# Kernel tuning notes

Measured on AMD Instinct MI355X. Metric: run time of the kernel, lower is better.

## Reference

```python
import jax, jax.numpy as jnp
import numpy as np

D_MODEL = 1024
NHEAD = 16
DK = D_MODEL // NHEAD
B, LQ, LK = 4, 2048, 2048


def setup_inputs() -> dict:
    key = jax.random.key(0)
    ks = jax.random.split(key, 11)
    s = 1.0 / np.sqrt(D_MODEL)
    inp = {
        "q": jax.random.normal(ks[0], (B, LQ, D_MODEL), jnp.float32),
        "k": jax.random.normal(ks[1], (B, LK, D_MODEL), jnp.float32),
        "v": jax.random.normal(ks[2], (B, LK, D_MODEL), jnp.float32),
        "attn_mask": jnp.triu(jnp.ones((LQ, LK), dtype=bool), k=1),  # True = masked (causal)
        "Wq": jax.random.normal(ks[3], (D_MODEL, D_MODEL), jnp.float32) * s,
        "bq": jnp.zeros((D_MODEL,), jnp.float32),
        "Wk": jax.random.normal(ks[4], (D_MODEL, D_MODEL), jnp.float32) * s,
        "bk": jnp.zeros((D_MODEL,), jnp.float32),
        "Wv": jax.random.normal(ks[5], (D_MODEL, D_MODEL), jnp.float32) * s,
        "bv": jnp.zeros((D_MODEL,), jnp.float32),
        "Wo": jax.random.normal(ks[6], (D_MODEL, D_MODEL), jnp.float32) * s,
        "bo": jnp.zeros((D_MODEL,), jnp.float32),
    }
    return inp


def _split_heads(x, L):
    # (B, L, D) -> (B, H, L, dk)
    return x.reshape(B, L, NHEAD, DK).transpose(0, 2, 1, 3)


def reference(q, k, v, attn_mask, Wq, bq, Wk, bk, Wv, bv, Wo, bo):
    qh = _split_heads(q @ Wq + bq, LQ)
    kh = _split_heads(k @ Wk + bk, LK)
    vh = _split_heads(v @ Wv + bv, LK)
    scale = 1.0 / np.sqrt(DK).astype(np.float32)
    scores = jnp.einsum("bhqd,bhkd->bhqk", qh, kh) * scale
    scores = jnp.where(attn_mask[None, None, :, :], -jnp.inf, scores)
    attn = jax.nn.softmax(scores, axis=-1)
    ctx = jnp.einsum("bhqk,bhkd->bhqd", attn, vh)
    ctx = ctx.transpose(0, 2, 1, 3).reshape(B, LQ, D_MODEL)
    return ctx @ Wo + bo
```

## Files before the change

kernel.cpp:

```cpp
#include <hip/hip_runtime.h>

#define D_MODEL 1024
#define NHEAD 16
#define DKH 64
#define BATCH 4
#define SEQ 2048
#define MROWS (BATCH*SEQ)

typedef unsigned short u16;
typedef __attribute__((ext_vector_type(8))) short bf16x8;
typedef __attribute__((ext_vector_type(4))) float f32x4;

__device__ __forceinline__ u16 f2bf(float f) {
  union { float f; unsigned int u; } x; x.f = f;
  unsigned int r = x.u + 0x7FFFu + ((x.u >> 16) & 1u);
  return (u16)(r >> 16);
}
__device__ __forceinline__ u16 f2bf_fast(float f) {
  union { float f; unsigned int u; } x; x.f = f;
  return (u16)((x.u + 0x7FFFu) >> 16);
}

__device__ __forceinline__ f32x4 mfma16(bf16x8 a, bf16x8 b, f32x4 c) {
  return __builtin_amdgcn_mfma_f32_16x16x32_bf16(a, b, c, 0, 0, 0);
}

__device__ __forceinline__ void gld_lds16(const void* g, void* l) {
  __builtin_amdgcn_global_load_lds((const __attribute__((address_space(1))) unsigned int*)g,
                                   (__attribute__((address_space(3))) unsigned int*)l, 16, 0, 0);
}

__global__ __launch_bounds__(256) void cvt3_kernel(
    const float* __restrict__ q, const float* __restrict__ k, const float* __restrict__ v,
    u16* __restrict__ oq, u16* __restrict__ ok, u16* __restrict__ ov) {
  const int seg = blockIdx.y;
  const float* in = (seg == 0) ? q : (seg == 1) ? k : v;
  u16* out = (seg == 0) ? oq : (seg == 1) ? ok : ov;
  int i = (blockIdx.x * 256 + threadIdx.x) * 4;
  float4 vv = *(const float4*)(in + i);
  ushort4 o;
  o.x = f2bf(vv.x); o.y = f2bf(vv.y); o.z = f2bf(vv.z); o.w = f2bf(vv.w);
  *(ushort4*)(out + i) = o;
}

__global__ __launch_bounds__(256) void transpose_cvt4(
    const float* __restrict__ W0, const float* __restrict__ W1,
    const float* __restrict__ W2, const float* __restrict__ W3,
    u16* __restrict__ T0, u16* __restrict__ T1,
    u16* __restrict__ T2, u16* __restrict__ T3) {
  const int z = blockIdx.z;
  const float* W = (z == 0) ? W0 : (z == 1) ? W1 : (z == 2) ? W2 : W3;
  u16* Wt = (z == 0) ? T0 : (z == 1) ? T1 : (z == 2) ? T2 : T3;
  __shared__ float tile[32][33];
  int bx = blockIdx.x * 32, by = blockIdx.y * 32;
  int tx = threadIdx.x, ty = threadIdx.y;
#pragma unroll
  for (int j = 0; j < 32; j += 8)
    tile[ty + j][tx] = W[(size_t)(by + ty + j) * D_MODEL + bx + tx];
  __syncthreads();
#pragma unroll
  for (int j = 0; j < 32; j += 8)
    Wt[(size_t)(bx + ty + j) * D_MODEL + by + tx] = f2bf(tile[tx][ty + j]);
}

__global__ __launch_bounds__(256, 2) void gemm_qkv_kernel(
    const u16* __restrict__ Aq, const u16* __restrict__ Ak, const u16* __restrict__ Av,
    const u16* __restrict__ Wt,
    const float* __restrict__ bq, const float* __restrict__ bk, const float* __restrict__ bv,
    u16* __restrict__ Qhd, u16* __restrict__ Khd, u16* __restrict__ Vhd, float qscale) {
  __shared__ u16 As[128 * 32];
  __shared__ u16 Bs[128 * 32];
  const int tid = threadIdx.x;
  const int lane = tid & 63;
  const int w = tid >> 6;
  const int wr = w >> 1, wc = w & 1;
  const int lo = lane & 15, g = lane >> 4;

  const int flat = blockIdx.x;
  const int swzb = (flat & 7) * 192 + (flat >> 3);
  const int m0 = (swzb / 24) * 128;
  const int n0 = (swzb % 24) * 128;
  const int chunk = n0 >> 10;
  const u16* A = (chunk == 0) ? Aq : (chunk == 1) ? Ak : Av;
  const float* bias = (chunk == 0) ? bq : (chunk == 1) ? bk : bv;
  const float scale = (chunk == 0) ? qscale : 1.0f;

  f32x4 acc[4][4] = {};

  for (int k0 = 0; k0 < D_MODEL; k0 += 32) {
#pragma unroll
    for (int cc = 0; cc < 2; ++cc) {
      int t = (w * 2 + cc) * 64 + lane;
      gld_lds16(A + (size_t)(m0 + (t >> 2)) * D_MODEL + k0 + (t & 3) * 8,
                As + (size_t)(w * 2 + cc) * 512);
      gld_lds16(Wt + (size_t)(n0 + (t >> 2)) * D_MODEL + k0 + (t & 3) * 8,
                Bs + (size_t)(w * 2 + cc) * 512);
    }
    __syncthreads();
    bf16x8 af[4], bf[4];
#pragma unroll
    for (int m = 0; m < 4; ++m)
      af[m] = *(const bf16x8*)&As[(wr * 64 + m * 16 + lo) * 32 + g * 8];
#pragma unroll
    for (int n = 0; n < 4; ++n)
      bf[n] = *(const bf16x8*)&Bs[(wc * 64 + n * 16 + lo) * 32 + g * 8];
#pragma unroll
    for (int m = 0; m < 4; ++m)
#pragma unroll
      for (int n = 0; n < 4; ++n)
        acc[m][n] = mfma16(af[m], bf[n], acc[m][n]);
    __syncthreads();
  }

#pragma unroll
  for (int m = 0; m < 4; ++m)
#pragma unroll
    for (int n = 0; n < 4; ++n) {
      int row0 = m0 + wr * 64 + m * 16 + g * 4;
      int colc = (n0 & 1023) + wc * 64 + n * 16 + lo;
      int hh = colc >> 6, d = colc & 63;
      int bb = row0 >> 11;
      float v0 = (acc[m][n][0] + bias[colc]) * scale;
      float v1 = (acc[m][n][1] + bias[colc]) * scale;
      float v2 = (acc[m][n][2] + bias[colc]) * scale;
      float v3 = (acc[m][n][3] + bias[colc]) * scale;
      if (chunk < 2) {
        u16* out = chunk ? Khd : Qhd;
#pragma unroll
        for (int i = 0; i < 4; ++i) {
          int l = (row0 + i) & 2047;
          float vi = (i == 0) ? v0 : (i == 1) ? v1 : (i == 2) ? v2 : v3;
          out[(((size_t)(bb * NHEAD + hh)) * SEQ + l) * DKH + d] = f2bf(vi);
        }
      } else {
        int l = row0 & 2047;
        int kh = (l >> 2) & 7;
        int pos = (l & ~31) | ((2 * (kh & 3) + (kh >> 2)) << 2);
        ushort4 o;
        o.x = f2bf(v0); o.y = f2bf(v1); o.z = f2bf(v2); o.w = f2bf(v3);
        *(ushort4*)&Vhd[(((size_t)(bb * NHEAD + hh)) * DKH + d) * SEQ + pos] = o;
      }
    }
}

__global__ __launch_bounds__(256, 2) void gemm_o_kernel(
    const u16* __restrict__ A, const u16* __restrict__ Bt,
    const float* __restrict__ bias, float* __restrict__ Cout) {
  __shared__ u16 As[128 * 32];
  __shared__ u16 Bs[128 * 32];
  const int tid = threadIdx.x;
  const int lane = tid & 63;
  const int w = tid >> 6;
  const int wr = w >> 1, wc = w & 1;
  const int lo = lane & 15, g = lane >> 4;

  const int flat = blockIdx.x;
  const int swzb = (flat & 7) * 64 + (flat >> 3);
  const int m0 = (swzb >> 3) * 128;
  const int n0 = (swzb & 7) * 128;

  f32x4 acc[4][4] = {};

  for (int k0 = 0; k0 < D_MODEL; k0 += 32) {
#pragma unroll
    for (int cc = 0; cc < 2; ++cc) {
      int t = (w * 2 + cc) * 64 + lane;
      gld_lds16(A + (size_t)(m0 + (t >> 2)) * D_MODEL + k0 + (t & 3) * 8,
                As + (size_t)(w * 2 + cc) * 512);
      gld_lds16(Bt + (size_t)(n0 + (t >> 2)) * D_MODEL + k0 + (t & 3) * 8,
                Bs + (size_t)(w * 2 + cc) * 512);
    }
    __syncthreads();
    bf16x8 af[4], bf[4];
#pragma unroll
    for (int m = 0; m < 4; ++m)
      af[m] = *(const bf16x8*)&As[(wr * 64 + m * 16 + lo) * 32 + g * 8];
#pragma unroll
    for (int n = 0; n < 4; ++n)
      bf[n] = *(const bf16x8*)&Bs[(wc * 64 + n * 16 + lo) * 32 + g * 8];
#pragma unroll
    for (int m = 0; m < 4; ++m)
#pragma unroll
      for (int n = 0; n < 4; ++n)
        acc[m][n] = mfma16(af[m], bf[n], acc[m][n]);
    __syncthreads();
  }

#pragma unroll
  for (int m = 0; m < 4; ++m)
#pragma unroll
    for (int n = 0; n < 4; ++n) {
      int row0 = m0 + wr * 64 + m * 16 + g * 4;
      int col = n0 + wc * 64 + n * 16 + lo;
#pragma unroll
      for (int i = 0; i < 4; ++i)
        Cout[(size_t)(row0 + i) * D_MODEL + col] = acc[m][n][i] + bias[col];
    }
}

__global__ __launch_bounds__(256, 3) void attn_kernel(
    const u16* __restrict__ Qh, const u16* __restrict__ Kh,
    const u16* __restrict__ Vt, u16* __restrict__ ctx) {
  const int blk = blockIdx.x;
  const int xcd = blk & 7;
  const int local = blk >> 3;
  const int qb = 15 - (local >> 3);
  const int head = xcd * 8 + (local & 7);
  const int b = head >> 4, h = head & (NHEAD - 1);

  const int tid = threadIdx.x;
  const int lane = tid & 63;
  const int w = tid >> 6;
  const int lo = lane & 15, g = lane >> 4;
  const int swz = (lo & 7) << 4;

  __shared__ u16 Ks[3][64 * 64];
  __shared__ u16 Vs[3][64 * 64];

  const size_t hoff = ((size_t)(b * NHEAD + h)) * SEQ * DKH;
  const u16* Qp = Qh + hoff;
  const u16* Kp = Kh + hoff;
  const u16* Vp = Vt + hoff;

  const int nt = 2 * qb + 2;
  const int qmin = qb * 128 + w * 32;

  bf16x8 aq[2][2];
#pragma unroll
  for (int qs = 0; qs < 2; ++qs)
#pragma unroll
    for (int cc = 0; cc < 2; ++cc)
      aq[qs][cc] = *(const bf16x8*)(Qp + (size_t)(qmin + qs * 16 + lo) * DKH + cc * 32 + g * 8);

  const int r_lo = lane >> 3;
  const int sgr = (lane & 7) ^ r_lo;

  auto STAGE = [&](int buf, int t64) {
#pragma unroll
    for (int j = 0; j < 2; ++j) {
      int row = w * 16 + j * 8 + r_lo;
      gld_lds16(Kp + (size_t)(t64 * 64 + row) * DKH + sgr * 8, &Ks[buf][(w * 2 + j) * 512]);
      gld_lds16(Vp + (size_t)row * SEQ + t64 * 64 + sgr * 8, &Vs[buf][(w * 2 + j) * 512]);
    }
  };

  STAGE(0, 0);
  STAGE(1, 1);
  asm volatile("s_waitcnt vmcnt(0)" ::: "memory");
  __builtin_amdgcn_s_barrier();

  f32x4 c[2][4] = {};
  float m_run[2] = {-1e30f, -1e30f}, l_run[2] = {0.f, 0.f};
  int cur = 0;

  for (int kt = 0; kt < nt; ++kt) {
    int b2 = cur + 2; if (b2 >= 3) b2 -= 3;
    if (kt + 2 < nt) STAGE(b2, kt + 2);

    f32x4 s[2][4] = {};
#pragma unroll
    for (int kn = 0; kn < 4; ++kn) {
      const char* krow = (const char*)&Ks[cur][(kn * 16 + lo) * 64];
#pragma unroll
      for (int cc = 0; cc < 2; ++cc) {
        bf16x8 ak = *(const bf16x8*)(krow + ((cc * 64 + g * 16) ^ swz));
        s[0][kn] = mfma16(ak, aq[0][cc], s[0][kn]);
        s[1][kn] = mfma16(ak, aq[1][cc], s[1][kn]);
      }
    }

    if (kt >= nt - 2) {
#pragma unroll
      for (int qs = 0; qs < 2; ++qs) {
        int q = qmin + qs * 16 + lo;
#pragma unroll
        for (int kn = 0; kn < 4; ++kn)
#pragma unroll
          for (int i = 0; i < 4; ++i) {
            int key = kt * 64 + kn * 16 + g * 4 + i;
            if (key > q) s[qs][kn][i] = -1e30f;
          }
      }
    }

    bf16x8 pb[2][2];
#pragma unroll
    for (int qs = 0; qs < 2; ++qs) {
      float mx = s[qs][0][0];
#pragma unroll
      for (int kn = 0; kn < 4; ++kn)
#pragma unroll
        for (int i = 0; i < 4; ++i) mx = fmaxf(mx, s[qs][kn][i]);
      mx = fmaxf(mx, __shfl_xor(mx, 16));
      mx = fmaxf(mx, __shfl_xor(mx, 32));
      float mnew = fmaxf(m_run[qs], mx);
      float al = __builtin_amdgcn_exp2f(m_run[qs] - mnew);
      m_run[qs] = mnew;
      float rs = 0.f;
#pragma unroll
      for (int kn = 0; kn < 4; ++kn)
#pragma unroll
        for (int i = 0; i < 4; ++i) {
          float p = __builtin_amdgcn_exp2f(s[qs][kn][i] - mnew);
          s[qs][kn][i] = p;
          rs += p;
        }
      rs += __shfl_xor(rs, 16);
      rs += __shfl_xor(rs, 32);
      l_run[qs] = l_run[qs] * al + rs;
#pragma unroll
      for (int dn = 0; dn < 4; ++dn) {
        c[qs][dn][0] *= al; c[qs][dn][1] *= al;
        c[qs][dn][2] *= al; c[qs][dn][3] *= al;
      }
#pragma unroll
      for (int kc = 0; kc < 2; ++kc) {
        bf16x8 t;
        t[0] = (short)f2bf_fast(s[qs][2 * kc][0]);
        t[1] = (short)f2bf_fast(s[qs][2 * kc][1]);
        t[2] = (short)f2bf_fast(s[qs][2 * kc][2]);
        t[3] = (short)f2bf_fast(s[qs][2 * kc][3]);
        t[4] = (short)f2bf_fast(s[qs][2 * kc + 1][0]);
        t[5] = (short)f2bf_fast(s[qs][2 * kc + 1][1]);
        t[6] = (short)f2bf_fast(s[qs][2 * kc + 1][2]);
        t[7] = (short)f2bf_fast(s[qs][2 * kc + 1][3]);
        pb[qs][kc] = t;
      }
    }

#pragma unroll
    for (int kc = 0; kc < 2; ++kc)
#pragma unroll
      for (int dn = 0; dn < 4; ++dn) {
        const char* vrow = (const char*)&Vs[cur][(dn * 16 + lo) * 64];
        bf16x8 av = *(const bf16x8*)(vrow + ((kc * 64 + g * 16) ^ swz));
        c[0][dn] = mfma16(av, pb[0][kc], c[0][dn]);
        c[1][dn] = mfma16(av, pb[1][kc], c[1][dn]);
      }

    if (kt + 1 < nt) {
      if (kt + 2 < nt) asm volatile("s_waitcnt vmcnt(4)" ::: "memory");
      else             asm volatile("s_waitcnt vmcnt(0)" ::: "memory");
      __builtin_amdgcn_s_barrier();
    }
    cur = (cur == 2) ? 0 : cur + 1;
  }

#pragma unroll
  for (int qs = 0; qs < 2; ++qs) {
    const float rl = 1.0f / l_run[qs];
    const int q = qmin + qs * 16 + lo;
#pragma unroll
    for (int dn = 0; dn < 4; ++dn) {
      ushort4 o;
      o.x = f2bf(c[qs][dn][0] * rl);
      o.y = f2bf(c[qs][dn][1] * rl);
      o.z = f2bf(c[qs][dn][2] * rl);
      o.w = f2bf(c[qs][dn][3] * rl);
      *(ushort4*)&ctx[((size_t)(b * SEQ + q)) * D_MODEL + h * DKH + dn * 16 + g * 4] = o;
    }
  }
}

extern "C" void kernel_launch(void* const* d_in, const int* in_sizes, int n_in,
                              void* d_out, int out_size, void* d_ws, size_t ws_size,
                              hipStream_t stream) {
  const float* q  = (const float*)d_in[0];
  const float* k  = (const float*)d_in[1];
  const float* v  = (const float*)d_in[2];
  const float* Wq = (const float*)d_in[4];
  const float* bq = (const float*)d_in[5];
  const float* Wk = (const float*)d_in[6];
  const float* bk = (const float*)d_in[7];
  const float* Wv = (const float*)d_in[8];
  const float* bv = (const float*)d_in[9];
  const float* Wo = (const float*)d_in[10];
  const float* bo = (const float*)d_in[11];

  char* ws = (char*)d_ws;
  const size_t MB = 1u << 20;
  u16* qb16 = (u16*)(ws + 0 * MB);
  u16* kb16 = (u16*)(ws + 16 * MB);
  u16* vb16 = (u16*)(ws + 32 * MB);
  u16* Wqkvt = (u16*)(ws + 48 * MB);
  u16* Wot  = (u16*)(ws + 54 * MB);
  u16* Qhd  = (u16*)(ws + 56 * MB);
  u16* Khd  = (u16*)(ws + 72 * MB);
  u16* Vhd  = (u16*)(ws + 88 * MB);
  u16* ctxb = qb16;

  cvt3_kernel<<<dim3(8192, 3), 256, 0, stream>>>(q, k, v, qb16, kb16, vb16);

  u16* Wqt = Wqkvt;
  u16* Wkt = Wqkvt + 1024 * 1024;
  u16* Wvt = Wqkvt + 2 * 1024 * 1024;
  transpose_cvt4<<<dim3(32, 32, 4), dim3(32, 8), 0, stream>>>(
      Wq, Wk, Wv, Wo, Wqt, Wkt, Wvt, Wot);

  const float qscale = 0.125f * 1.4426950408889634f;
  gemm_qkv_kernel<<<1536, 256, 0, stream>>>(qb16, kb16, vb16, Wqkvt,
                                            bq, bk, bv, Qhd, Khd, Vhd, qscale);

  attn_kernel<<<1024, 256, 0, stream>>>(Qhd, Khd, Vhd, ctxb);

  gemm_o_kernel<<<512, 256, 0, stream>>>(ctxb, Wot, bo, (float*)d_out);
}
```

Baseline: 187.1 us.

## Pipeline projection GEMMs with double-buffered swizzled LDS and split MFMA phases

```diff
diff --git a/kernel.cpp b/kernel.cpp
--- a/kernel.cpp
+++ b/kernel.cpp
@@ -63,139 +63,176 @@
     Wt[(size_t)(bx + ty + j) * D_MODEL + by + tx] = f2bf(tile[tx][ty + j]);
 }
 
+template <typename Epi>
+__device__ __forceinline__ void gemm_pipe(const u16* __restrict__ Ap,
+                                          const u16* __restrict__ Bp,
+                                          int m0, int n0g, Epi epi) {
+  __shared__ u16 As[2][128 * 64];
+  __shared__ u16 Bs[2][128 * 64];
+  const int tid = threadIdx.x;
+  const int lane = tid & 63;
+  const int w = tid >> 6;
+  const int wm = w >> 1, wn = w & 1;
+  const int lo = lane & 15, g = lane >> 4;
+  const int swz = (lo & 7) << 4;
+  const int sg = (tid & 7) ^ ((tid >> 3) & 7);
+  const int srow = tid >> 3;
+
+  f32x4 acc[4][4] = {};
+
+  auto STAGE_A = [&](int buf, int tt, int j) {
+    int row = j * 32 + srow;
+    gld_lds16(Ap + (size_t)(m0 + row) * D_MODEL + tt * 64 + sg * 8,
+              &As[buf][j * 2048 + tid * 8]);
+  };
+  auto STAGE_B = [&](int buf, int tt, int j) {
+    int row = j * 32 + srow;
+    gld_lds16(Bp + (size_t)(n0g + row) * D_MODEL + tt * 64 + sg * 8,
+              &Bs[buf][j * 2048 + tid * 8]);
+  };
+
+  STAGE_A(0, 0, 0); STAGE_A(0, 0, 1); STAGE_A(0, 0, 2); STAGE_A(0, 0, 3);
+  STAGE_B(0, 0, 0); STAGE_B(0, 0, 1); STAGE_B(0, 0, 2); STAGE_B(0, 0, 3);
+  STAGE_B(1, 1, 0); STAGE_B(1, 1, 1); STAGE_B(1, 1, 2); STAGE_B(1, 1, 3);
+  asm volatile("s_waitcnt vmcnt(4)" ::: "memory");
+  __builtin_amdgcn_s_barrier();
+
+  int cur = 0;
+#pragma unroll 1
+  for (int t = 0; t < 16; ++t) {
+    const int nb = cur ^ 1;
+    const char* ab = (const char*)&As[cur][0];
+    const char* bb2 = (const char*)&Bs[cur][0];
+
+    bf16x8 bf[4][2], af[2][2];
+#pragma unroll
+    for (int n = 0; n < 4; ++n) {
+      int row = wn * 64 + n * 16 + lo;
+      bf[n][0] = *(const bf16x8*)(bb2 + row * 128 + ((g * 16) ^ swz));
+      bf[n][1] = *(const bf16x8*)(bb2 + row * 128 + ((64 + g * 16) ^ swz));
+    }
+#pragma unroll
+    for (int m = 0; m < 2; ++m) {
+      int row = wm * 64 + m * 16 + lo;
+      af[m][0] = *(const bf16x8*)(ab + row * 128 + ((g * 16) ^ swz));
+      af[m][1] = *(const bf16x8*)(ab + row * 128 + ((64 + g * 16) ^ swz));
+    }
+    if (t + 1 < 16) {
+      STAGE_A(nb, t + 1, 0); STAGE_A(nb, t + 1, 1);
+      STAGE_A(nb, t + 1, 2); STAGE_A(nb, t + 1, 3);
+    }
+    __builtin_amdgcn_s_barrier();
+    __builtin_amdgcn_s_setprio(1);
+#pragma unroll
+    for (int s2 = 0; s2 < 2; ++s2)
+#pragma unroll
+      for (int m = 0; m < 2; ++m)
+#pragma unroll
+        for (int n = 0; n < 4; ++n)
+          acc[m][n] = mfma16(af[m][s2], bf[n][s2], acc[m][n]);
+    __builtin_amdgcn_s_setprio(0);
+    __builtin_amdgcn_s_barrier();
+
+    bf16x8 af2[2][2];
+#pragma unroll
+    for (int m = 0; m < 2; ++m) {
+      int row = wm * 64 + (m + 2) * 16 + lo;
+      af2[m][0] = *(const bf16x8*)(ab + row * 128 + ((g * 16) ^ swz));
+      af2[m][1] = *(const bf16x8*)(ab + row * 128 + ((64 + g * 16) ^ swz));
+    }
+    if (t + 2 < 16) {
+      STAGE_B(cur, t + 2, 0); STAGE_B(cur, t + 2, 1);
+      STAGE_B(cur, t + 2, 2); STAGE_B(cur, t + 2, 3);
+    }
+    __builtin_amdgcn_s_barrier();
+    __builtin_amdgcn_s_setprio(1);
+#pragma unroll
+    for (int s2 = 0; s2 < 2; ++s2)
+#pragma unroll
+      for (int m = 0; m < 2; ++m)
+#pragma unroll
+        for (int n = 0; n < 4; ++n)
+          acc[m + 2][n] = mfma16(af2[m][s2], bf[n][s2], acc[m + 2][n]);
+    __builtin_amdgcn_s_setprio(0);
+    if (t + 2 < 16) asm volatile("s_waitcnt vmcnt(4)" ::: "memory");
+    else            asm volatile("s_waitcnt vmcnt(0)" ::: "memory");
+    __builtin_amdgcn_s_barrier();
+    cur = nb;
+  }
+
+  epi(acc, wm, wn, lo, g);
+}
+
 __global__ __launch_bounds__(256, 2) void gemm_qkv_kernel(
     const u16* __restrict__ Aq, const u16* __restrict__ Ak, const u16* __restrict__ Av,
     const u16* __restrict__ Wt,
     const float* __restrict__ bq, const float* __restrict__ bk, const float* __restrict__ bv,
     u16* __restrict__ Qhd, u16* __restrict__ Khd, u16* __restrict__ Vhd, float qscale) {
-  __shared__ u16 As[128 * 32];
-  __shared__ u16 Bs[128 * 32];
-  const int tid = threadIdx.x;
-  const int lane = tid & 63;
-  const int w = tid >> 6;
-  const int wr = w >> 1, wc = w & 1;
-  const int lo = lane & 15, g = lane >> 4;
-
   const int flat = blockIdx.x;
   const int swzb = (flat & 7) * 192 + (flat >> 3);
   const int m0 = (swzb / 24) * 128;
-  const int n0 = (swzb % 24) * 128;
-  const int chunk = n0 >> 10;
-  const u16* A = (chunk == 0) ? Aq : (chunk == 1) ? Ak : Av;
+  const int n0g = (swzb % 24) * 128;
+  const int chunk = n0g >> 10;
+  const u16* Ap = (chunk == 0) ? Aq : (chunk == 1) ? Ak : Av;
   const float* bias = (chunk == 0) ? bq : (chunk == 1) ? bk : bv;
   const float scale = (chunk == 0) ? qscale : 1.0f;
 
-  f32x4 acc[4][4] = {};
-
-  for (int k0 = 0; k0 < D_MODEL; k0 += 32) {
-#pragma unroll
-    for (int cc = 0; cc < 2; ++cc) {
-      int t = (w * 2 + cc) * 64 + lane;
-      gld_lds16(A + (size_t)(m0 + (t >> 2)) * D_MODEL + k0 + (t & 3) * 8,
-                As + (size_t)(w * 2 + cc) * 512);
-      gld_lds16(Wt + (size_t)(n0 + (t >> 2)) * D_MODEL + k0 + (t & 3) * 8,
-                Bs + (size_t)(w * 2 + cc) * 512);
-    }
-    __syncthreads();
-    bf16x8 af[4], bf[4];
-#pragma unroll
-    for (int m = 0; m < 4; ++m)
-      af[m] = *(const bf16x8*)&As[(wr * 64 + m * 16 + lo) * 32 + g * 8];
-#pragma unroll
-    for (int n = 0; n < 4; ++n)
-      bf[n] = *(const bf16x8*)&Bs[(wc * 64 + n * 16 + lo) * 32 + g * 8];
-#pragma unroll
-    for (int m = 0; m < 4; ++m)
-#pragma unroll
-      for (int n = 0; n < 4; ++n)
-        acc[m][n] = mfma16(af[m], bf[n], acc[m][n]);
-    __syncthreads();
-  }
-
-#pragma unroll
-  for (int m = 0; m < 4; ++m)
-#pragma unroll
-    for (int n = 0; n < 4; ++n) {
-      int row0 = m0 + wr * 64 + m * 16 + g * 4;
-      int colc = (n0 & 1023) + wc * 64 + n * 16 + lo;
-      int hh = colc >> 6, d = colc & 63;
-      int bb = row0 >> 11;
-      float v0 = (acc[m][n][0] + bias[colc]) * scale;
-      float v1 = (acc[m][n][1] + bias[colc]) * scale;
-      float v2 = (acc[m][n][2] + bias[colc]) * scale;
-      float v3 = (acc[m][n][3] + bias[colc]) * scale;
-      if (chunk < 2) {
-        u16* out = chunk ? Khd : Qhd;
-#pragma unroll
-        for (int i = 0; i < 4; ++i) {
-          int l = (row0 + i) & 2047;
-          float vi = (i == 0) ? v0 : (i == 1) ? v1 : (i == 2) ? v2 : v3;
-          out[(((size_t)(bb * NHEAD + hh)) * SEQ + l) * DKH + d] = f2bf(vi);
+  gemm_pipe(Ap, Wt, m0, n0g,
+    [&](f32x4 (&acc)[4][4], int wm, int wn, int lo, int g) {
+#pragma unroll
+      for (int m = 0; m < 4; ++m)
+#pragma unroll
+        for (int n = 0; n < 4; ++n) {
+          int row0 = m0 + wm * 64 + m * 16 + g * 4;
+          int colc = (n0g & 1023) + wn * 64 + n * 16 + lo;
+          int hh = colc >> 6, d = colc & 63;
+          int bb = row0 >> 11;
+          float v0 = (acc[m][n][0] + bias[colc]) * scale;
+          float v1 = (acc[m][n][1] + bias[colc]) * scale;
+          float v2 = (acc[m][n][2] + bias[colc]) * scale;
+          float v3 = (acc[m][n][3] + bias[colc]) * scale;
+          if (chunk < 2) {
+            u16* out = chunk ? Khd : Qhd;
+#pragma unroll
+            for (int i = 0; i < 4; ++i) {
+              int l = (row0 + i) & 2047;
+              float vi = (i == 0) ? v0 : (i == 1) ? v1 : (i == 2) ? v2 : v3;
+              out[(((size_t)(bb * NHEAD + hh)) * SEQ + l) * DKH + d] = f2bf(vi);
+            }
+          } else {
+            int l = row0 & 2047;
+            int kh = (l >> 2) & 7;
+            int pos = (l & ~31) | ((2 * (kh & 3) + (kh >> 2)) << 2);
+            ushort4 o;
+            o.x = f2bf(v0); o.y = f2bf(v1); o.z = f2bf(v2); o.w = f2bf(v3);
+            *(ushort4*)&Vhd[(((size_t)(bb * NHEAD + hh)) * DKH + d) * SEQ + pos] = o;
+          }
         }
-      } else {
-        int l = row0 & 2047;
-        int kh = (l >> 2) & 7;
-        int pos = (l & ~31) | ((2 * (kh & 3) + (kh >> 2)) << 2);
-        ushort4 o;
-        o.x = f2bf(v0); o.y = f2bf(v1); o.z = f2bf(v2); o.w = f2bf(v3);
-        *(ushort4*)&Vhd[(((size_t)(bb * NHEAD + hh)) * DKH + d) * SEQ + pos] = o;
-      }
-    }
+    });
 }
 
 __global__ __launch_bounds__(256, 2) void gemm_o_kernel(
     const u16* __restrict__ A, const u16* __restrict__ Bt,
     const float* __restrict__ bias, float* __restrict__ Cout) {
-  __shared__ u16 As[128 * 32];
-  __shared__ u16 Bs[128 * 32];
-  const int tid = threadIdx.x;
-  const int lane = tid & 63;
-  const int w = tid >> 6;
-  const int wr = w >> 1, wc = w & 1;
-  const int lo = lane & 15, g = lane >> 4;
-
   const int flat = blockIdx.x;
   const int swzb = (flat & 7) * 64 + (flat >> 3);
   const int m0 = (swzb >> 3) * 128;
-  const int n0 = (swzb & 7) * 128;
-
-  f32x4 acc[4][4] = {};
-
-  for (int k0 = 0; k0 < D_MODEL; k0 += 32) {
-#pragma unroll
-    for (int cc = 0; cc < 2; ++cc) {
-      int t = (w * 2 + cc) * 64 + lane;
-      gld_lds16(A + (size_t)(m0 + (t >> 2)) * D_MODEL + k0 + (t & 3) * 8,
-                As + (size_t)(w * 2 + cc) * 512);
-      gld_lds16(Bt + (size_t)(n0 + (t >> 2)) * D_MODEL + k0 + (t & 3) * 8,
-                Bs + (size_t)(w * 2 + cc) * 512);
-    }
-    __syncthreads();
-    bf16x8 af[4], bf[4];
-#pragma unroll
-    for (int m = 0; m < 4; ++m)
-      af[m] = *(const bf16x8*)&As[(wr * 64 + m * 16 + lo) * 32 + g * 8];
-#pragma unroll
-    for (int n = 0; n < 4; ++n)
-      bf[n] = *(const bf16x8*)&Bs[(wc * 64 + n * 16 + lo) * 32 + g * 8];
-#pragma unroll
-    for (int m = 0; m < 4; ++m)
-#pragma unroll
-      for (int n = 0; n < 4; ++n)
-        acc[m][n] = mfma16(af[m], bf[n], acc[m][n]);
-    __syncthreads();
-  }
-
-#pragma unroll
-  for (int m = 0; m < 4; ++m)
-#pragma unroll
-    for (int n = 0; n < 4; ++n) {
-      int row0 = m0 + wr * 64 + m * 16 + g * 4;
-      int col = n0 + wc * 64 + n * 16 + lo;
-#pragma unroll
-      for (int i = 0; i < 4; ++i)
-        Cout[(size_t)(row0 + i) * D_MODEL + col] = acc[m][n][i] + bias[col];
-    }
+  const int n0g = (swzb & 7) * 128;
+
+  gemm_pipe(A, Bt, m0, n0g,
+    [&](f32x4 (&acc)[4][4], int wm, int wn, int lo, int g) {
+#pragma unroll
+      for (int m = 0; m < 4; ++m)
+#pragma unroll
+        for (int n = 0; n < 4; ++n) {
+          int row0 = m0 + wm * 64 + m * 16 + g * 4;
+          int col = n0g + wn * 64 + n * 16 + lo;
+          float bcol = bias[col];
+#pragma unroll
+          for (int i = 0; i < 4; ++i)
+            Cout[(size_t)(row0 + i) * D_MODEL + col] = acc[m][n][i] + bcol;
+        }
+    });
 }
 
 __global__ __launch_bounds__(256, 3) void attn_kernel(
```

New measurement: 177.4 us. 5.2% less time.
